# Performance work log

Hardware: AMD Instinct MI355X
Metric: run time of the kernel (lower is better)

## Reference

```python
import jax, jax.numpy as jnp
import numpy as np

B, S, H = 8, 2048, 512

def setup_inputs() -> dict:
    key = jax.random.key(0)
    k1, k2, k3 = jax.random.split(key, 3)
    O = jax.random.normal(k1, (B, S, H), dtype=jnp.float32)
    # torch Linear default init ~ U(-1/sqrt(H), 1/sqrt(H)); scale randn similarly
    Wa_w = jax.random.normal(k2, (H, H), dtype=jnp.float32) / jnp.sqrt(jnp.float32(H))
    Wa_b = jax.random.normal(k3, (H,), dtype=jnp.float32) / jnp.sqrt(jnp.float32(H))
    return {"O": O, "Wa_w": Wa_w, "Wa_b": Wa_b}

def reference(O, Wa_w, Wa_b):
    # Q = tanh(O @ Wa_w^T + b)   (torch Linear convention: y = x W^T + b)
    Q = jnp.tanh(jnp.einsum('bsh,oh->bso', O, Wa_w) + Wa_b)
    # scores = Q @ O^T  -> (B, S, S)
    scores = jnp.einsum('bsh,bth->bst', Q, O)
    a = jax.nn.softmax(scores, axis=-1)
    # Oa = a @ O -> (B, S, H)
    Oa = jnp.einsum('bst,bth->bsh', a, O)
    return Oa
```

## Files before the change

kernel.cpp:

```cpp
#include <hip/hip_runtime.h>
#include <cmath>

typedef _Float16 f16;
typedef _Float16 f16x8 __attribute__((ext_vector_type(8)));
typedef float    f32x4 __attribute__((ext_vector_type(4)));
typedef unsigned short u16;
typedef unsigned int   u32;
typedef u16 us8 __attribute__((ext_vector_type(8)));
typedef u16 us4 __attribute__((ext_vector_type(4)));

#define MFMA16(a, b, c) __builtin_amdgcn_mfma_f32_16x16x32_f16((a), (b), (c), 0, 0, 0)

__device__ __forceinline__ void gload_lds16(const void* g, void* l) {
    __builtin_amdgcn_global_load_lds((const __attribute__((address_space(1))) void*)g,
                                     (__attribute__((address_space(3))) void*)l, 16, 0, 0);
}

__global__ void castk(const float* __restrict__ src, f16* __restrict__ dst, int n8) {
    int i = blockIdx.x * 256 + threadIdx.x;
    if (i >= n8) return;
    const float4* s = (const float4*)src + (size_t)i * 2;
    float4 a = s[0], b = s[1];
    union { f16 h[8]; us8 v; } o;
    o.h[0] = (f16)a.x; o.h[1] = (f16)a.y; o.h[2] = (f16)a.z; o.h[3] = (f16)a.w;
    o.h[4] = (f16)b.x; o.h[5] = (f16)b.y; o.h[6] = (f16)b.z; o.h[7] = (f16)b.w;
    *(us8*)&dst[(size_t)i * 8] = o.v;
}

__global__ void transpose_cast(const float* __restrict__ O, f16* __restrict__ OT) {
    __shared__ f16 tbuf[64][68];
    int bid = blockIdx.x;
    int b = bid >> 8, t = bid & 255;
    int s0 = (t & 31) * 64, h0 = (t >> 5) * 64;
    const float* Ob = O + (size_t)b * 2048 * 512;
    f16* OTb = OT + (size_t)b * 512 * 2048;
    int tid = threadIdx.x;
    int rr = tid >> 4, cc = (tid & 15) * 4;
#pragma unroll
    for (int i = 0; i < 4; ++i) {
        int r = rr + 16 * i;
        float4 v = *(const float4*)&Ob[(size_t)(s0 + r) * 512 + h0 + cc];
        tbuf[r][cc + 0] = (f16)v.x; tbuf[r][cc + 1] = (f16)v.y;
        tbuf[r][cc + 2] = (f16)v.z; tbuf[r][cc + 3] = (f16)v.w;
    }
    __syncthreads();
#pragma unroll
    for (int i = 0; i < 4; ++i) {
        int hr = rr + 16 * i;
        union { f16 h[4]; us4 v; } pk;
        pk.h[0] = tbuf[cc + 0][hr]; pk.h[1] = tbuf[cc + 1][hr];
        pk.h[2] = tbuf[cc + 2][hr]; pk.h[3] = tbuf[cc + 3][hr];
        *(us4*)&OTb[(size_t)(h0 + hr) * 2048 + s0 + cc] = pk.v;
    }
}

__global__ __launch_bounds__(256) void gemm1(const f16* __restrict__ A,
                                             const f16* __restrict__ W,
                                             const float* __restrict__ bias,
                                             f16* __restrict__ Qo) {
    __shared__ f16 lA[128 * 32];
    __shared__ f16 lB[128 * 32];
    const int tid = threadIdx.x;
    const int lane = tid & 63, w = tid >> 6;
    const int wm = w >> 1, wn = w & 1;
    const int bm = blockIdx.x >> 2, bn = blockIdx.x & 3;
    const int r0 = bm * 128, c0 = bn * 128;
    const int l15 = lane & 15, g = lane >> 4;
    f32x4 acc[4][4] = {};
    for (int kt = 0; kt < 16; ++kt) {
        int k0 = kt * 32;
        __syncthreads();
#pragma unroll
        for (int i = 0; i < 2; ++i) {
            int slot = i * 256 + tid;
            int row = slot >> 2, oct = slot & 3;
            int soct = oct ^ (row & 3);
            *(us8*)&lA[slot * 8] = *(const us8*)&A[(size_t)(r0 + row) * 512 + k0 + soct * 8];
            *(us8*)&lB[slot * 8] = *(const us8*)&W[(size_t)(c0 + row) * 512 + k0 + soct * 8];
        }
        __syncthreads();
        f16x8 af[4], bf[4];
#pragma unroll
        for (int mf = 0; mf < 4; ++mf) {
            int row = 64 * wm + 16 * mf + l15;
            int oct = g ^ (row & 3);
            af[mf] = *(const f16x8*)&lA[(row * 4 + oct) * 8];
        }
#pragma unroll
        for (int nf = 0; nf < 4; ++nf) {
            int row = 64 * wn + 16 * nf + l15;
            int oct = g ^ (row & 3);
            bf[nf] = *(const f16x8*)&lB[(row * 4 + oct) * 8];
        }
#pragma unroll
        for (int mf = 0; mf < 4; ++mf)
#pragma unroll
            for (int nf = 0; nf < 4; ++nf)
                acc[mf][nf] = MFMA16(af[mf], bf[nf], acc[mf][nf]);
    }
    float bv[4];
#pragma unroll
    for (int nf = 0; nf < 4; ++nf) bv[nf] = bias[c0 + 64 * wn + 16 * nf + l15];
#pragma unroll
    for (int mf = 0; mf < 4; ++mf) {
#pragma unroll
        for (int nf = 0; nf < 4; ++nf) {
#pragma unroll
            for (int r = 0; r < 4; ++r) {
                float y = tanhf(acc[mf][nf][r] + bv[nf]);
                int row = r0 + 64 * wm + 16 * mf + 4 * g + r;
                int col = c0 + 64 * wn + 16 * nf + l15;
                Qo[(size_t)row * 512 + col] = (f16)y;
            }
        }
    }
}

__global__ __launch_bounds__(512, 2) void attn(const f16* __restrict__ Qf,
                                               const f16* __restrict__ Of,
                                               const f16* __restrict__ OfT,
                                               float* __restrict__ P0,
                                               f16* __restrict__ P1,
                                               float* __restrict__ ML) {
    extern __shared__ __align__(16) char smem[];
    const int tid = threadIdx.x;
    const int lane = tid & 63, w = tid >> 6;
    const int l15 = lane & 15, g = lane >> 4;
    const int b = blockIdx.x & 7, tt = (blockIdx.x >> 3) & 1, qt = blockIdx.x >> 4;
    const int q0 = qt * 128;
    const int tb = tt * 1024;
    const f16* Ob  = Of  + (size_t)b * 2048 * 512;
    const f16* OTb = OfT + (size_t)b * 512 * 2048;

    f16x8 qf[16];
    const f16* qrow = Qf + ((size_t)b * 2048 + q0 + 16 * w + l15) * 512;
#pragma unroll
    for (int ks = 0; ks < 16; ++ks) qf[ks] = *(const f16x8*)&qrow[ks * 32 + g * 8];

    float m = -INFINITY, lsum = 0.f;
    f32x4 acc[32] = {};

    const int addrA = 4 * (32 * (g & 1) + l15);
    const int addrB = addrA + 64;
    const int kx = (l15 & 3) ^ ((l15 >> 2) & 3);
    const int go = g ^ kx;

    auto STAGE_K = [&](int buf, int t0) {
        f16* dst = (f16*)(smem + buf * 32768);
#pragma unroll
        for (int i = 0; i < 4; ++i) {
            int slot = i * 512 + tid;
            int t = slot >> 6, oct = slot & 63;
            gload_lds16(&Ob[(size_t)(t0 + t) * 512 + 8 * (oct ^ (t & 7))], &dst[slot * 8]);
        }
    };
    auto STAGE_V = [&](int buf, int t0) {
        f16* dst = (f16*)(smem + 65536 + buf * 32768);
#pragma unroll
        for (int i = 0; i < 4; ++i) {
            int slot = i * 512 + tid;
            int h = slot >> 2, gr = slot & 3;
            int key = (h & 3) ^ ((h >> 2) & 3);
            gload_lds16(&OTb[(size_t)h * 2048 + t0 + 8 * (gr ^ key)], &dst[slot * 8]);
        }
    };

    STAGE_K(0, tb);
    STAGE_V(0, tb);

    for (int kt = 0; kt < 32; ++kt) {
        const int cur = kt & 1;
        const f16* lK = (const f16*)(smem + cur * 32768);
        const f16* lV = (const f16*)(smem + 65536 + cur * 32768);

        if (kt < 31) {
            STAGE_K(cur ^ 1, tb + (kt + 1) * 32);
            STAGE_V(cur ^ 1, tb + (kt + 1) * 32);
            asm volatile("s_waitcnt vmcnt(8)" ::: "memory");
        } else {
            asm volatile("s_waitcnt vmcnt(0)" ::: "memory");
        }
        __builtin_amdgcn_s_barrier();

        f32x4 sa[2] = {};
#pragma unroll
        for (int ks = 0; ks < 16; ++ks) {
#pragma unroll
            for (int mf = 0; mf < 2; ++mf) {
                int t = 16 * mf + l15;
                int oct = (4 * ks + g) ^ (t & 7);
                f16x8 kf = *(const f16x8*)&lK[(t * 64 + oct) * 8];
                sa[mf] = MFMA16(kf, qf[ks], sa[mf]);
            }
        }

        float tmax = -INFINITY;
#pragma unroll
        for (int mf = 0; mf < 2; ++mf)
#pragma unroll
            for (int r = 0; r < 4; ++r) tmax = fmaxf(tmax, sa[mf][r]);
        tmax = fmaxf(tmax, __shfl_xor(tmax, 16));
        tmax = fmaxf(tmax, __shfl_xor(tmax, 32));
        if (__any(tmax > m + 8.0f)) {
            float mnew = fmaxf(m, tmax);
            float corr = __expf(m - mnew);
            m = mnew;
            lsum *= corr;
#pragma unroll
            for (int hf = 0; hf < 32; ++hf) acc[hf] *= corr;
        }
        float p[2][4];
        float ps = 0.f;
#pragma unroll
        for (int mf = 0; mf < 2; ++mf)
#pragma unroll
            for (int r = 0; r < 4; ++r) { p[mf][r] = __expf(sa[mf][r] - m); ps += p[mf][r]; }
        ps += __shfl_xor(ps, 16);
        ps += __shfl_xor(ps, 32);
        lsum += ps;

        u32 Wd[2][2];
#pragma unroll
        for (int mf = 0; mf < 2; ++mf)
#pragma unroll
            for (int c = 0; c < 2; ++c) {
                union { f16 h[2]; u32 u; } x;
                x.h[0] = (f16)p[mf][2 * c]; x.h[1] = (f16)p[mf][2 * c + 1];
                Wd[mf][c] = x.u;
            }
        u32 word[4];
#pragma unroll
        for (int pp = 0; pp < 4; ++pp) {
            int adr = (pp >> 1) ? addrB : addrA;
            int w0 = __builtin_amdgcn_ds_bpermute(adr, (int)Wd[0][pp & 1]);
            int w1 = __builtin_amdgcn_ds_bpermute(adr, (int)Wd[1][pp & 1]);
            word[pp] = (lane >= 32) ? (u32)w1 : (u32)w0;
        }
        union { u32 u[4]; f16x8 v; } pkk;
        pkk.u[0] = word[0]; pkk.u[1] = word[1]; pkk.u[2] = word[2]; pkk.u[3] = word[3];
        f16x8 pfrag = pkk.v;

#pragma unroll
        for (int hf = 0; hf < 32; ++hf) {
            int h = 16 * hf + l15;
            f16x8 vf = *(const f16x8*)&lV[(h * 4 + go) * 8];
            acc[hf] = MFMA16(vf, pfrag, acc[hf]);
        }

        asm volatile("s_waitcnt lgkmcnt(0)" ::: "memory");
        __builtin_amdgcn_s_barrier();
    }

    const size_t row = (size_t)b * 2048 + q0 + 16 * w + l15;
    if (g == 0) {
        ML[(tt * 16384 + row) * 2 + 0] = m;
        ML[(tt * 16384 + row) * 2 + 1] = lsum;
    }
    if (tt == 0) {
#pragma unroll
        for (int hf = 0; hf < 32; ++hf) {
            float4 o;
            o.x = acc[hf][0]; o.y = acc[hf][1];
            o.z = acc[hf][2]; o.w = acc[hf][3];
            *(float4*)&P0[row * 512 + 16 * hf + 4 * g] = o;
        }
    } else {
        float inv = 1.0f / lsum;
#pragma unroll
        for (int hf = 0; hf < 32; ++hf) {
            union { f16 h[4]; us4 v; } pk;
            pk.h[0] = (f16)(acc[hf][0] * inv); pk.h[1] = (f16)(acc[hf][1] * inv);
            pk.h[2] = (f16)(acc[hf][2] * inv); pk.h[3] = (f16)(acc[hf][3] * inv);
            *(us4*)&P1[row * 512 + 16 * hf + 4 * g] = pk.v;
        }
    }
}

__global__ __launch_bounds__(256) void merge_k(float* __restrict__ P0,
                                               const f16* __restrict__ P1,
                                               const float* __restrict__ ML) {
    const int tid = threadIdx.x;
    const size_t row = (size_t)blockIdx.x * 8 + (tid >> 5);
    const int c = (tid & 31) * 16;
    float m0 = ML[row * 2 + 0], l0 = ML[row * 2 + 1];
    float m1 = ML[(16384 + row) * 2 + 0], l1 = ML[(16384 + row) * 2 + 1];
    float M = fmaxf(m0, m1);
    float e0 = __expf(m0 - M), e1 = __expf(m1 - M);
    float w1 = e1 * l1;
    float inv = 1.0f / (e0 * l0 + w1);
    float a0 = e0 * inv, a1 = w1 * inv;
#pragma unroll
    for (int j = 0; j < 4; ++j) {
        size_t off = row * 512 + c + 4 * j;
        float4 v0 = *(const float4*)&P0[off];
        us4 v1u = *(const us4*)&P1[off];
        const f16* v1 = (const f16*)&v1u;
        float4 o;
        o.x = a0 * v0.x + a1 * (float)v1[0];
        o.y = a0 * v0.y + a1 * (float)v1[1];
        o.z = a0 * v0.z + a1 * (float)v1[2];
        o.w = a0 * v0.w + a1 * (float)v1[3];
        *(float4*)&P0[off] = o;
    }
}

extern "C" void kernel_launch(void* const* d_in, const int* in_sizes, int n_in,
                              void* d_out, int out_size, void* d_ws, size_t ws_size,
                              hipStream_t stream) {
    const float* O  = (const float*)d_in[0];
    const float* Ww = (const float*)d_in[1];
    const float* Wb = (const float*)d_in[2];
    float* Out = (float*)d_out;
    char* ws = (char*)d_ws;
    f16* Of16 = (f16*)ws;
    f16* OT   = (f16*)(ws + ((size_t)16 << 20));
    f16* Qf   = (f16*)(ws + ((size_t)32 << 20));
    f16* Wf   = (f16*)(ws + ((size_t)48 << 20));
    f16* P1   = (f16*)(ws + ((size_t)49 << 20));
    float* ML = (float*)(ws + ((size_t)65 << 20));

    hipFuncSetAttribute((const void*)attn, hipFuncAttributeMaxDynamicSharedMemorySize, 131072);

    castk<<<4096, 256, 0, stream>>>(O, Of16, 1048576);
    castk<<<128, 256, 0, stream>>>(Ww, Wf, 32768);
    transpose_cast<<<2048, 256, 0, stream>>>(O, OT);
    gemm1<<<512, 256, 0, stream>>>(Of16, Wf, Wb, Qf);
    attn<<<256, 512, 131072, stream>>>(Qf, Of16, OT, Out, P1, ML);
    merge_k<<<2048, 256, 0, stream>>>(Out, P1, ML);
}
```

Baseline: 176.3 us.

## Share P tile through LDS so each wave computes a 64-column slice of PV

The attention kernel no longer has each wave accumulate all 512 output columns for its own 16 query rows. Each wave now writes its softmax probabilities and rescale factors to LDS, and after a barrier computes a 64-wide column slice of the PV product for all 128 query rows. This cuts the per-wave V-fragment LDS reads by a factor of eight, at the cost of an extra barrier per tile, more LDS (occupancy drops to one block per CU), and an unconditional per-step rescale of the accumulators. It also fuses the fp16 cast of O into the transpose kernel, removing one pass over the input.

```diff
diff --git a/kernel.cpp b/kernel.cpp
--- a/kernel.cpp
+++ b/kernel.cpp
@@ -6,6 +6,7 @@
 typedef float    f32x4 __attribute__((ext_vector_type(4)));
 typedef unsigned short u16;
 typedef unsigned int   u32;
+typedef unsigned long long u64;
 typedef u16 us8 __attribute__((ext_vector_type(8)));
 typedef u16 us4 __attribute__((ext_vector_type(4)));
 
@@ -27,12 +28,14 @@
     *(us8*)&dst[(size_t)i * 8] = o.v;
 }
 
-__global__ void transpose_cast(const float* __restrict__ O, f16* __restrict__ OT) {
+__global__ void prep(const float* __restrict__ O, f16* __restrict__ Of16,
+                     f16* __restrict__ OT) {
     __shared__ f16 tbuf[64][68];
     int bid = blockIdx.x;
     int b = bid >> 8, t = bid & 255;
     int s0 = (t & 31) * 64, h0 = (t >> 5) * 64;
     const float* Ob = O + (size_t)b * 2048 * 512;
+    f16* Ofb = Of16 + (size_t)b * 2048 * 512;
     f16* OTb = OT + (size_t)b * 512 * 2048;
     int tid = threadIdx.x;
     int rr = tid >> 4, cc = (tid & 15) * 4;
@@ -40,8 +43,11 @@
     for (int i = 0; i < 4; ++i) {
         int r = rr + 16 * i;
         float4 v = *(const float4*)&Ob[(size_t)(s0 + r) * 512 + h0 + cc];
-        tbuf[r][cc + 0] = (f16)v.x; tbuf[r][cc + 1] = (f16)v.y;
-        tbuf[r][cc + 2] = (f16)v.z; tbuf[r][cc + 3] = (f16)v.w;
+        union { f16 h[4]; us4 u; } st;
+        st.h[0] = (f16)v.x; st.h[1] = (f16)v.y; st.h[2] = (f16)v.z; st.h[3] = (f16)v.w;
+        *(us4*)&Ofb[(size_t)(s0 + r) * 512 + h0 + cc] = st.u;
+        tbuf[r][cc + 0] = st.h[0]; tbuf[r][cc + 1] = st.h[1];
+        tbuf[r][cc + 2] = st.h[2]; tbuf[r][cc + 3] = st.h[3];
     }
     __syncthreads();
 #pragma unroll
@@ -116,13 +122,16 @@
     }
 }
 
-__global__ __launch_bounds__(512, 2) void attn(const f16* __restrict__ Qf,
+__global__ __launch_bounds__(512, 1) void attn(const f16* __restrict__ Qf,
                                                const f16* __restrict__ Of,
                                                const f16* __restrict__ OfT,
                                                float* __restrict__ P0,
                                                f16* __restrict__ P1,
                                                float* __restrict__ ML) {
     extern __shared__ __align__(16) char smem[];
+    f16*   lP    = (f16*)(smem + 131072);
+    float* lcorr = (float*)(smem + 139264);
+    float* linv  = (float*)(smem + 139776);
     const int tid = threadIdx.x;
     const int lane = tid & 63, w = tid >> 6;
     const int l15 = lane & 15, g = lane >> 4;
@@ -138,12 +147,12 @@
     for (int ks = 0; ks < 16; ++ks) qf[ks] = *(const f16x8*)&qrow[ks * 32 + g * 8];
 
     float m = -INFINITY, lsum = 0.f;
-    f32x4 acc[32] = {};
-
-    const int addrA = 4 * (32 * (g & 1) + l15);
-    const int addrB = addrA + 64;
+    f32x4 acc[4][8] = {};
+
+    const int pkey = (l15 >> 1) & 3;
     const int kx = (l15 & 3) ^ ((l15 >> 2) & 3);
     const int go = g ^ kx;
+    const int qloc = 16 * w + l15;
 
     auto STAGE_K = [&](int buf, int t0) {
         f16* dst = (f16*)(smem + buf * 32768);
@@ -201,14 +210,9 @@
             for (int r = 0; r < 4; ++r) tmax = fmaxf(tmax, sa[mf][r]);
         tmax = fmaxf(tmax, __shfl_xor(tmax, 16));
         tmax = fmaxf(tmax, __shfl_xor(tmax, 32));
-        if (__any(tmax > m + 8.0f)) {
-            float mnew = fmaxf(m, tmax);
-            float corr = __expf(m - mnew);
-            m = mnew;
-            lsum *= corr;
-#pragma unroll
-            for (int hf = 0; hf < 32; ++hf) acc[hf] *= corr;
-        }
+        float mnew = fmaxf(m, tmax);
+        float corr = __expf(m - mnew);
+        m = mnew;
         float p[2][4];
         float ps = 0.f;
 #pragma unroll
@@ -217,61 +221,70 @@
             for (int r = 0; r < 4; ++r) { p[mf][r] = __expf(sa[mf][r] - m); ps += p[mf][r]; }
         ps += __shfl_xor(ps, 16);
         ps += __shfl_xor(ps, 32);
-        lsum += ps;
-
-        u32 Wd[2][2];
-#pragma unroll
-        for (int mf = 0; mf < 2; ++mf)
-#pragma unroll
-            for (int c = 0; c < 2; ++c) {
-                union { f16 h[2]; u32 u; } x;
-                x.h[0] = (f16)p[mf][2 * c]; x.h[1] = (f16)p[mf][2 * c + 1];
-                Wd[mf][c] = x.u;
-            }
-        u32 word[4];
-#pragma unroll
-        for (int pp = 0; pp < 4; ++pp) {
-            int adr = (pp >> 1) ? addrB : addrA;
-            int w0 = __builtin_amdgcn_ds_bpermute(adr, (int)Wd[0][pp & 1]);
-            int w1 = __builtin_amdgcn_ds_bpermute(adr, (int)Wd[1][pp & 1]);
-            word[pp] = (lane >= 32) ? (u32)w1 : (u32)w0;
-        }
-        union { u32 u[4]; f16x8 v; } pkk;
-        pkk.u[0] = word[0]; pkk.u[1] = word[1]; pkk.u[2] = word[2]; pkk.u[3] = word[3];
-        f16x8 pfrag = pkk.v;
-
-#pragma unroll
-        for (int hf = 0; hf < 32; ++hf) {
-            int h = 16 * hf + l15;
-            f16x8 vf = *(const f16x8*)&lV[(h * 4 + go) * 8];
-            acc[hf] = MFMA16(vf, pfrag, acc[hf]);
-        }
+        lsum = lsum * corr + ps;
+        if (g == 0) lcorr[qloc] = corr;
+
+        union { f16 h[4]; u64 u; } pk0, pk1;
+#pragma unroll
+        for (int r = 0; r < 4; ++r) { pk0.h[r] = (f16)p[0][r]; pk1.h[r] = (f16)p[1][r]; }
+        *(u64*)((char*)lP + qloc * 64 + 16 * (((g >> 1)    ) ^ pkey) + 8 * (g & 1)) = pk0.u;
+        *(u64*)((char*)lP + qloc * 64 + 16 * (((g >> 1) + 2) ^ pkey) + 8 * (g & 1)) = pk1.u;
 
         asm volatile("s_waitcnt lgkmcnt(0)" ::: "memory");
         __builtin_amdgcn_s_barrier();
-    }
-
-    const size_t row = (size_t)b * 2048 + q0 + 16 * w + l15;
+
+        f16x8 vf[4];
+#pragma unroll
+        for (int hf = 0; hf < 4; ++hf) {
+            int h = 64 * w + 16 * hf + l15;
+            vf[hf] = *(const f16x8*)&lV[(h * 4 + go) * 8];
+        }
+#pragma unroll
+        for (int qfi = 0; qfi < 8; ++qfi) {
+            float c = lcorr[16 * qfi + l15];
+            f16x8 pf = *(const f16x8*)((const char*)lP + (16 * qfi + l15) * 64 + 16 * (g ^ pkey));
+#pragma unroll
+            for (int hf = 0; hf < 4; ++hf) {
+                acc[hf][qfi] *= c;
+                acc[hf][qfi] = MFMA16(vf[hf], pf, acc[hf][qfi]);
+            }
+        }
+
+        asm volatile("s_waitcnt lgkmcnt(0)" ::: "memory");
+        __builtin_amdgcn_s_barrier();
+    }
+
     if (g == 0) {
-        ML[(tt * 16384 + row) * 2 + 0] = m;
-        ML[(tt * 16384 + row) * 2 + 1] = lsum;
-    }
+        const size_t mrow = (size_t)tt * 16384 + (size_t)b * 2048 + q0 + qloc;
+        ML[mrow * 2 + 0] = m;
+        ML[mrow * 2 + 1] = lsum;
+        linv[qloc] = 1.0f / lsum;
+    }
+    __syncthreads();
     if (tt == 0) {
 #pragma unroll
-        for (int hf = 0; hf < 32; ++hf) {
-            float4 o;
-            o.x = acc[hf][0]; o.y = acc[hf][1];
-            o.z = acc[hf][2]; o.w = acc[hf][3];
-            *(float4*)&P0[row * 512 + 16 * hf + 4 * g] = o;
+        for (int qfi = 0; qfi < 8; ++qfi) {
+            const size_t row = (size_t)b * 2048 + q0 + 16 * qfi + l15;
+#pragma unroll
+            for (int hf = 0; hf < 4; ++hf) {
+                float4 o;
+                o.x = acc[hf][qfi][0]; o.y = acc[hf][qfi][1];
+                o.z = acc[hf][qfi][2]; o.w = acc[hf][qfi][3];
+                *(float4*)&P0[row * 512 + 64 * w + 16 * hf + 4 * g] = o;
+            }
         }
     } else {
-        float inv = 1.0f / lsum;
-#pragma unroll
-        for (int hf = 0; hf < 32; ++hf) {
-            union { f16 h[4]; us4 v; } pk;
-            pk.h[0] = (f16)(acc[hf][0] * inv); pk.h[1] = (f16)(acc[hf][1] * inv);
-            pk.h[2] = (f16)(acc[hf][2] * inv); pk.h[3] = (f16)(acc[hf][3] * inv);
-            *(us4*)&P1[row * 512 + 16 * hf + 4 * g] = pk.v;
+#pragma unroll
+        for (int qfi = 0; qfi < 8; ++qfi) {
+            const size_t row = (size_t)b * 2048 + q0 + 16 * qfi + l15;
+            float inv = linv[16 * qfi + l15];
+#pragma unroll
+            for (int hf = 0; hf < 4; ++hf) {
+                union { f16 h[4]; us4 v; } pk;
+                pk.h[0] = (f16)(acc[hf][qfi][0] * inv); pk.h[1] = (f16)(acc[hf][qfi][1] * inv);
+                pk.h[2] = (f16)(acc[hf][qfi][2] * inv); pk.h[3] = (f16)(acc[hf][qfi][3] * inv);
+                *(us4*)&P1[row * 512 + 64 * w + 16 * hf + 4 * g] = pk.v;
+            }
         }
     }
 }
@@ -319,12 +332,11 @@
     f16* P1   = (f16*)(ws + ((size_t)49 << 20));
     float* ML = (float*)(ws + ((size_t)65 << 20));
 
-    hipFuncSetAttribute((const void*)attn, hipFuncAttributeMaxDynamicSharedMemorySize, 131072);
-
-    castk<<<4096, 256, 0, stream>>>(O, Of16, 1048576);
+    hipFuncSetAttribute((const void*)attn, hipFuncAttributeMaxDynamicSharedMemorySize, 140288);
+
+    prep<<<2048, 256, 0, stream>>>(O, Of16, OT);
     castk<<<128, 256, 0, stream>>>(Ww, Wf, 32768);
-    transpose_cast<<<2048, 256, 0, stream>>>(O, OT);
     gemm1<<<512, 256, 0, stream>>>(Of16, Wf, Wb, Qf);
-    attn<<<256, 512, 131072, stream>>>(Qf, Of16, OT, Out, P1, ML);
+    attn<<<256, 512, 140288, stream>>>(Qf, Of16, OT, Out, P1, ML);
     merge_k<<<2048, 256, 0, stream>>>(Out, P1, ML);
 }
```

Result: slower. 196.2 us (+11.3%).
